# Kernel optimization log

Measured on AMD Instinct MI355X. Metric: run time of the kernel, lower is better.

Reference implementation:

```python
import jax, jax.numpy as jnp
import numpy as np

N, E, IN, H, O, ED = 20000, 100000, 167, 4, 256, 10
HID = H * O  # 1024
BN_EPS = 1e-5


def _bn(x, g, b):
    # BatchNorm1d in training mode: batch statistics over nodes
    mu = x.mean(0)
    var = x.var(0)
    return (x - mu) * jax.lax.rsqrt(var + BN_EPS) * g + b


def _gat(x, src, dst, ef, Wg, We, attn, at, cb, heads, out):
    # modified_GAT: multi-head attention with edge features + time scalar
    n = x.shape[0]
    h = (x @ Wg).reshape(n, heads, out)                 # [N,H,O]
    e = (ef[:, 1:] @ We).reshape(-1, heads, out)        # [E,H,O] edge-feature proj
    t = ef[:, 0]                                        # [E] time feature
    # node-level attention scores (avoids materializing [E,H,O] twice)
    s_src = jnp.einsum('nhd,hd->nh', h, attn[0])
    s_dst = jnp.einsum('nhd,hd->nh', h, attn[1])
    s_e = jnp.einsum('ehd,hd->eh', e, attn[2])
    logits = jax.nn.leaky_relu(s_src[src] + s_dst[dst] + s_e + t[:, None] * at, 0.2)  # [E,H]
    # attention normalization: softmax over incoming edges of each dst node
    m = jax.ops.segment_max(logits, dst, num_segments=n)
    m = jnp.where(jnp.isfinite(m), m, 0.0)
    p = jnp.exp(logits - m[dst])
    denom = jax.ops.segment_sum(p, dst, num_segments=n)
    w = p / (denom[dst] + 1e-16)                        # [E,H]
    msg = w[:, :, None] * (h[src] + e)                  # [E,H,O]
    agg = jax.ops.segment_sum(msg, dst, num_segments=n) # [N,H,O]
    return agg.reshape(n, heads * out) + cb


def setup_inputs() -> dict:
    key = jax.random.key(0)
    ks = iter(jax.random.split(key, 64))

    def nrm(shape, s):
        return jax.random.normal(next(ks), shape, dtype=jnp.float32) * np.float32(s)

    d = {}
    d['x'] = jax.random.normal(next(ks), (N, IN), dtype=jnp.float32)
    d['edge_index'] = jax.random.randint(next(ks), (2, E), 0, N)
    d['edge_attr'] = jax.random.uniform(next(ks), (E, ED + 2), dtype=jnp.float32)
    conv_dims = [(IN, H, O), (HID, H, O), (HID, 1, 2)]
    for i, (fin, hh, oo) in enumerate(conv_dims, 1):
        d[f'Wg{i}'] = nrm((fin, hh * oo), 1.0 / np.sqrt(fin))
        d[f'We{i}'] = nrm((ED, hh * oo), 1.0 / np.sqrt(ED))
        d[f'attn{i}'] = nrm((3, hh, oo), 0.1)
        d[f'at{i}'] = nrm((hh,), 0.1)
        d[f'cb{i}'] = jnp.zeros((hh * oo,), jnp.float32)
    lin_dims = [(IN, HID), (HID, HID), (HID, 2)]
    bn_dims = [IN, HID, HID]
    for i, (fin, fo) in enumerate(lin_dims, 1):
        d[f'lw{i}'] = nrm((fin, fo), 1.0 / np.sqrt(fin))
        d[f'lb{i}'] = jnp.zeros((fo,), jnp.float32)
        d[f'g{i}'] = jnp.ones((bn_dims[i - 1],), jnp.float32)
        d[f'b{i}'] = jnp.zeros((bn_dims[i - 1],), jnp.float32)
    return d


def reference(x, edge_index, edge_attr,
              Wg1, We1, attn1, at1, cb1, lw1, lb1, g1, b1,
              Wg2, We2, attn2, at2, cb2, lw2, lb2, g2, b2,
              Wg3, We3, attn3, at3, cb3, lw3, lb3, g3, b3):
    src, dst = edge_index[0], edge_index[1]
    ef = edge_attr[:, :-1]  # drop edge class column
    h = _bn(x, g1, b1)
    h = jax.nn.relu(h @ lw1 + lb1 + _gat(h, src, dst, ef, Wg1, We1, attn1, at1, cb1, H, O))
    h = _bn(h, g2, b2)
    h = jax.nn.relu(h @ lw2 + lb2 + _gat(h, src, dst, ef, Wg2, We2, attn2, at2, cb2, H, O))
    h = _bn(h, g3, b3)
    h = jax.nn.relu(h @ lw3 + lb3 + _gat(h, src, dst, ef, Wg3, We3, attn3, at3, cb3, 1, 2))
    return h
```

## Files before the change

kernel.cpp:

```cpp
#include <hip/hip_runtime.h>
#include <math.h>

#define NN 20000
#define EE 100000
#define FIN 167
#define KP1 256
#define HID 1024
#define OO 256
#define NB 16

typedef unsigned short u16;
typedef short bf16x8 __attribute__((ext_vector_type(8)));
typedef short s16x4  __attribute__((ext_vector_type(4)));
typedef float f32x4  __attribute__((ext_vector_type(4)));

__device__ __forceinline__ float bf(u16 u){ return __uint_as_float(((unsigned)u)<<16); }
__device__ __forceinline__ u16 fb(float v){
  unsigned u = __float_as_uint(v);
  return (u16)((u + 0x7FFFu + ((u>>16)&1u)) >> 16);
}
__device__ __forceinline__ float ldv(const float* p, long i){ return p[i]; }
__device__ __forceinline__ float ldv(const u16*   p, long i){ return bf(p[i]); }

__global__ void k_count(const int* __restrict__ ei, int* __restrict__ counts){
  int e = blockIdx.x*256 + threadIdx.x;
  if (e < EE) atomicAdd(&counts[ei[EE+e]], 1);
}

__global__ __launch_bounds__(256) void k_scan(const int* __restrict__ counts, int* __restrict__ iptr){
  __shared__ int sd[256];
  int tid = threadIdx.x;
  int carry = 0;
  for (int base=0; base<NN; base+=256){
    int i = base+tid;
    int v = (i<NN)? counts[i] : 0;
    sd[tid]=v;
    __syncthreads();
    for (int off=1; off<256; off<<=1){
      int t = (tid>=off)? sd[tid-off] : 0;
      __syncthreads();
      sd[tid] += t;
      __syncthreads();
    }
    if (i<NN) iptr[i] = carry + sd[tid] - v;
    carry += sd[255];
    __syncthreads();
  }
  if (tid==0) iptr[NN]=carry;
}

__global__ void k_fill(const int* __restrict__ ei, const int* __restrict__ iptr,
                       int* __restrict__ cursor, int* __restrict__ eid){
  int e = blockIdx.x*256 + threadIdx.x;
  if (e < EE){
    int d = ei[EE+e];
    int pos = atomicAdd(&cursor[d],1);
    eid[iptr[d]+pos] = e;
  }
}

template<typename T>
__global__ void k_bnstats(const T* __restrict__ X, float* __restrict__ sums, int F){
  int f = blockIdx.y*256 + threadIdx.x;
  if (f >= F) return;
  int r0 = blockIdx.x*100, r1 = r0+100;
  float s=0.f, s2=0.f;
  for (int r=r0;r<r1;r++){ float v = ldv(X,(long)r*F+f); s += v; s2 += v*v; }
  atomicAdd(&sums[f], s);
  atomicAdd(&sums[F+f], s2);
}

__global__ __launch_bounds__(256) void k_bnstats8(const u16* __restrict__ X, float* __restrict__ part){
  int tid = threadIdx.x;
  int f8 = (tid & 127)*8;
  int r0 = blockIdx.x*79, r1 = min(NN, r0+79);
  float s[8]={0,0,0,0,0,0,0,0}, s2[8]={0,0,0,0,0,0,0,0};
  for (int r=r0 + (tid>>7); r<r1; r+=2){
    bf16x8 v = *(const bf16x8*)(X + (long)r*HID + f8);
    #pragma unroll
    for (int j=0;j<8;j++){ float x=bf((u16)v[j]); s[j]+=x; s2[j]+=x*x; }
  }
  __shared__ float red[256][8];
  float* pb = part + (long)blockIdx.x*2048;
  #pragma unroll
  for (int j=0;j<8;j++) red[tid][j]=s[j];
  __syncthreads();
  if (tid<128){
    #pragma unroll
    for (int j=0;j<8;j++) pb[f8+j] = red[tid][j]+red[tid+128][j];
  }
  __syncthreads();
  #pragma unroll
  for (int j=0;j<8;j++) red[tid][j]=s2[j];
  __syncthreads();
  if (tid<128){
    #pragma unroll
    for (int j=0;j<8;j++) pb[1024+f8+j] = red[tid][j]+red[tid+128][j];
  }
}

__global__ __launch_bounds__(256) void k_pred(const float* __restrict__ part, float* __restrict__ sums){
  int idx = blockIdx.x*256 + threadIdx.x;
  float s = 0.f;
  #pragma unroll 8
  for (int b=0;b<256;b++) s += part[(long)b*2048 + idx];
  sums[idx] = s;
}

__global__ void k_bnfin(const float* __restrict__ sums, const float* __restrict__ g,
                        const float* __restrict__ b, float* __restrict__ scale,
                        float* __restrict__ shift, int F){
  int f = blockIdx.x*256 + threadIdx.x;
  if (f >= F) return;
  float mu  = sums[f]   * (1.f/NN);
  float var = sums[F+f] * (1.f/NN) - mu*mu;
  float sc  = rsqrtf(var + 1e-5f) * g[f];
  scale[f] = sc;
  shift[f] = b[f] - mu*sc;
}

__global__ __launch_bounds__(256) void k_foldT(const float* __restrict__ Wg, const float* __restrict__ Wl,
                        const float* __restrict__ scale,
                        u16* __restrict__ Wt, int K, int Kp){
  __shared__ float t[32][33];
  int k0 = blockIdx.x*32, c0 = blockIdx.y*32;
  int tx = threadIdx.x & 31, ty = threadIdx.x >> 5;
  bool second = (c0 >= HID);
  const float* W = second ? Wl : Wg;
  int cc0 = second ? c0 - HID : c0;
  #pragma unroll
  for (int i=0;i<4;i++){
    int k = k0 + ty + i*8;
    t[ty+i*8][tx] = (k < K) ? W[(long)k*HID + cc0 + tx] * scale[k] : 0.f;
  }
  __syncthreads();
  #pragma unroll
  for (int i=0;i<4;i++){
    int c = c0 + ty + i*8;
    Wt[(long)c*Kp + k0 + tx] = fb(t[tx][ty+i*8]);
  }
}

__global__ void k_cinit(const float* __restrict__ lb, float* __restrict__ cst){
  int c = blockIdx.x*256 + threadIdx.x;
  if (c < 2*HID) cst[c] = (c >= HID) ? lb[c-HID] : 0.f;
}

__global__ __launch_bounds__(256) void k_const(const float* __restrict__ Wg, const float* __restrict__ Wl,
                        const float* __restrict__ shift, float* __restrict__ cst, int K){
  int tx = threadIdx.x & 63, ty = threadIdx.x >> 6;
  int c = blockIdx.x*64 + tx;
  bool second = c >= HID;
  const float* W = second ? Wl : Wg;
  int cc = second ? c-HID : c;
  int k0 = blockIdx.y*128;
  int k1 = min(K, k0+128);
  float s = 0.f;
  for (int k=k0+ty; k<k1; k+=4) s += shift[k]*W[(long)k*HID+cc];
  __shared__ float red[256];
  red[threadIdx.x] = s;
  __syncthreads();
  if (ty == 0){
    float tot = red[tx] + red[tx+64] + red[tx+128] + red[tx+192];
    atomicAdd(&cst[c], tot);
  }
}

__global__ void k_cast(const float* __restrict__ x, u16* __restrict__ xb){
  long idx = (long)blockIdx.x*256 + threadIdx.x;
  if (idx >= (long)NN*KP1) return;
  int n = (int)(idx / KP1), k = (int)(idx % KP1);
  xb[idx] = (k<FIN)? fb(x[(long)n*FIN+k]) : (u16)0;
}

__global__ void k_we16(const float* __restrict__ We, u16* __restrict__ We16){
  int i = blockIdx.x*256 + threadIdx.x;
  if (i < 10*HID) We16[i] = fb(We[i]);
}

#define MF(a_,b_,c_) __builtin_amdgcn_mfma_f32_16x16x32_bf16(a_,b_,c_,0,0,0)
#define FENCE asm volatile("" ::: "memory")
#define BAR do { FENCE; __builtin_amdgcn_s_barrier(); FENCE; } while(0)

__global__ __launch_bounds__(512,2) void k_gemm(const u16* __restrict__ A, int K,
                     const u16* __restrict__ Wt, const float* __restrict__ cst,
                     u16* __restrict__ Chg, u16* __restrict__ Clin){
  __shared__ u16 lds[2][24576];
  int b = blockIdx.x;
  int wg = (b & 7)*158 + (b >> 3);
  int row0 = (wg >> 4)*256, col0 = (wg & 15)*128;
  int tid = threadIdx.x;
  int wave = tid >> 6, lane = tid & 63, quad = lane >> 4, lo = lane & 15;
  int wm = wave >> 1, wn = wave & 1;
  const u16* Apt[2];
  #pragma unroll
  for (int i=0;i<2;i++){
    int s = i*512 + tid, srow = s>>2;
    int gr = row0 + srow; if (gr >= NN) gr = NN-1;
    Apt[i] = A + (long)gr*K + (((s&3)^(srow&3))*8);
  }
  int brow = tid>>2;
  const u16* Bpt = Wt + (long)(col0 + brow)*K + ((((tid&3)^(brow&3)))*8);
  const char* ldsc = (const char*)&lds[0][0];
  int axor = lo & 3;
  int aoff = (wm*64 + lo)*64 + ((quad^axor)*16);
  int boff = 32768 + (wn*64 + lo)*64 + ((quad^axor)*16);
  int NT = K >> 6;
  f32x4 acc[4][4] = {};
  {
    u16* d = (u16*)&lds[0][0];
    __builtin_amdgcn_global_load_lds(Apt[0],      d +          tid*8, 16, 0, 0);
    __builtin_amdgcn_global_load_lds(Apt[1],      d +  4096 +  tid*8, 16, 0, 0);
    __builtin_amdgcn_global_load_lds(Bpt,         d + 16384 +  tid*8, 16, 0, 0);
    __builtin_amdgcn_global_load_lds(Apt[0] + 32, d +  8192 +  tid*8, 16, 0, 0);
    __builtin_amdgcn_global_load_lds(Apt[1] + 32, d + 12288 +  tid*8, 16, 0, 0);
    __builtin_amdgcn_global_load_lds(Bpt    + 32, d + 20480 +  tid*8, 16, 0, 0);
    asm volatile("s_waitcnt vmcnt(3)" ::: "memory");
    BAR;
  }
  for (int t=0; t<NT; t++){
    const char* Lb = ldsc + (t&1)*49152;
    u16* Sb = (u16*)&lds[0][0] + ((t&1)^1)*24576;
    int k0n = (t+1) << 6;
    int nx = (t+1 < NT);
    bf16x8 af[4], bfr[4];
    #pragma unroll
    for (int i=0;i<4;i++) af[i]  = *(const bf16x8*)(Lb + aoff + i*1024);
    #pragma unroll
    for (int n=0;n<4;n++) bfr[n] = *(const bf16x8*)(Lb + boff + n*1024);
    if (nx){
      __builtin_amdgcn_global_load_lds(Apt[0] + k0n, Sb +          tid*8, 16, 0, 0);
      __builtin_amdgcn_global_load_lds(Apt[1] + k0n, Sb +  4096 +  tid*8, 16, 0, 0);
      __builtin_amdgcn_global_load_lds(Bpt    + k0n, Sb + 16384 +  tid*8, 16, 0, 0);
    }
    #pragma unroll
    for (int i=0;i<4;i++)
      #pragma unroll
      for (int n=0;n<4;n++)
        acc[i][n] = MF(af[i], bfr[n], acc[i][n]);
    if (nx) asm volatile("s_waitcnt vmcnt(3)" ::: "memory");
    else    asm volatile("s_waitcnt vmcnt(0)" ::: "memory");
    BAR;
    #pragma unroll
    for (int i=0;i<4;i++) af[i]  = *(const bf16x8*)(Lb + 16384 + aoff + i*1024);
    #pragma unroll
    for (int n=0;n<4;n++) bfr[n] = *(const bf16x8*)(Lb +  8192 + boff + n*1024);
    if (nx){
      __builtin_amdgcn_global_load_lds(Apt[0] + k0n + 32, Sb +  8192 +  tid*8, 16, 0, 0);
      __builtin_amdgcn_global_load_lds(Apt[1] + k0n + 32, Sb + 12288 +  tid*8, 16, 0, 0);
      __builtin_amdgcn_global_load_lds(Bpt    + k0n + 32, Sb + 20480 +  tid*8, 16, 0, 0);
    }
    #pragma unroll
    for (int i=0;i<4;i++)
      #pragma unroll
      for (int n=0;n<4;n++)
        acc[i][n] = MF(af[i], bfr[n], acc[i][n]);
    if (nx) asm volatile("s_waitcnt vmcnt(3)" ::: "memory");
    BAR;
  }
  #pragma unroll
  for (int i=0;i<4;i++){
    #pragma unroll
    for (int n=0;n<4;n++){
      int col = col0 + wn*64 + n*16 + lo;
      float cs = cst[col];
      #pragma unroll
      for (int r=0;r<4;r++){
        int row = row0 + wm*64 + i*16 + quad*4 + r;
        if (row < NN){
          u16 o = fb(acc[i][n][r] + cs);
          if (col < HID) Chg[(long)row*HID + col] = o;
          else           Clin[(long)row*HID + col - HID] = o;
        }
      }
    }
  }
}
#undef MF
#undef BAR
#undef FENCE

__global__ __launch_bounds__(256) void k_sdot(const u16* __restrict__ hg, const float* __restrict__ attn,
                       float* __restrict__ ssrc, float* __restrict__ sdst){
  int unit = blockIdx.x*4 + (threadIdx.x >> 6);
  if (unit >= NN*4) return;
  int lane = threadIdx.x & 63;
  int n = unit >> 2, h = unit & 3;
  const u16* hp = hg + (long)n*HID + h*OO + lane*4;
  s16x4 v = *(const s16x4*)hp;
  float4 x0 = *(const float4*)(attn + h*OO + lane*4);
  float4 x1 = *(const float4*)(attn + HID + h*OO + lane*4);
  float f0 = bf((u16)v.x), f1 = bf((u16)v.y), f2 = bf((u16)v.z), f3 = bf((u16)v.w);
  float ss = f0*x0.x + f1*x0.y + f2*x0.z + f3*x0.w;
  float sd = f0*x1.x + f1*x1.y + f2*x1.z + f3*x1.w;
  #pragma unroll
  for (int off=32; off>0; off>>=1){
    ss += __shfl_down(ss, off);
    sd += __shfl_down(sd, off);
  }
  if (lane==0){ ssrc[unit]=ss; sdst[unit]=sd; }
}

__global__ void k_q(const float* __restrict__ We, const float* __restrict__ attn,
                    float* __restrict__ q){
  int t = threadIdx.x;
  if (t >= 40) return;
  int k = t >> 2, h = t & 3;
  float s = 0.f;
  for (int d=0; d<OO; d++) s += We[(long)k*HID + h*OO + d] * attn[2*HID + h*OO + d];
  q[k*4+h] = s;
}

__global__ void k_logits(const int* __restrict__ ei, const float* __restrict__ ea,
                         const float* __restrict__ q, const float* __restrict__ at,
                         const float* __restrict__ ssrc, const float* __restrict__ sdst,
                         float* __restrict__ L){
  int e = blockIdx.x*256 + threadIdx.x;
  if (e >= EE) return;
  int s = ei[e], dd = ei[EE+e];
  float4 a0 = *(const float4*)(ea + (long)e*12);
  float4 a1 = *(const float4*)(ea + (long)e*12 + 4);
  float4 a2 = *(const float4*)(ea + (long)e*12 + 8);
  float t = a0.x;
  float cc[10] = {a0.y,a0.z,a0.w, a1.x,a1.y,a1.z,a1.w, a2.x,a2.y,a2.z};
  float4 ss = *(const float4*)(ssrc + (long)s*4);
  float4 sd = *(const float4*)(sdst + (long)dd*4);
  float sv[4] = {ss.x+sd.x, ss.y+sd.y, ss.z+sd.z, ss.w+sd.w};
  float4 out;
  #pragma unroll
  for (int h=0;h<4;h++){
    float se = 0.f;
    #pragma unroll
    for (int k=0;k<10;k++) se += cc[k]*q[k*4+h];
    float v = sv[h] + se + t*at[h];
    ((float*)&out)[h] = (v>0.f)? v : 0.2f*v;
  }
  *(float4*)(L + (long)e*4) = out;
}

__global__ void k_mden(const int* __restrict__ iptr, const int* __restrict__ eid,
                       const float* __restrict__ ea, float* __restrict__ L,
                       float* __restrict__ cw){
  int n = blockIdx.x*256 + threadIdx.x;
  if (n >= NN) return;
  int b = iptr[n], e1 = iptr[n+1];
  float m0=-INFINITY, m1=-INFINITY, m2=-INFINITY, m3=-INFINITY;
  for (int i=b;i<e1;i++){
    float4 l = *(const float4*)(L + (long)eid[i]*4);
    m0=fmaxf(m0,l.x); m1=fmaxf(m1,l.y); m2=fmaxf(m2,l.z); m3=fmaxf(m3,l.w);
  }
  if (b==e1){ m0=m1=m2=m3=0.f; }
  float s0=0.f,s1=0.f,s2=0.f,s3=0.f;
  for (int i=b;i<e1;i++){
    float4 l = *(const float4*)(L + (long)eid[i]*4);
    s0+=expf(l.x-m0); s1+=expf(l.y-m1); s2+=expf(l.z-m2); s3+=expf(l.w-m3);
  }
  float d0=1.f/(s0+1e-16f), d1=1.f/(s1+1e-16f), d2=1.f/(s2+1e-16f), d3=1.f/(s3+1e-16f);
  float c[4][10] = {};
  for (int i=b;i<e1;i++){
    int e = eid[i];
    float4 l = *(const float4*)(L + (long)e*4);
    float4 w = { expf(l.x-m0)*d0, expf(l.y-m1)*d1, expf(l.z-m2)*d2, expf(l.w-m3)*d3 };
    *(float4*)(L + (long)e*4) = w;
    float4 a0 = *(const float4*)(ea + (long)e*12);
    float4 a1 = *(const float4*)(ea + (long)e*12 + 4);
    float4 a2 = *(const float4*)(ea + (long)e*12 + 8);
    float cc[10] = {a0.y,a0.z,a0.w, a1.x,a1.y,a1.z,a1.w, a2.x,a2.y,a2.z};
    #pragma unroll
    for (int k=0;k<10;k++){
      c[0][k] += w.x*cc[k]; c[1][k] += w.y*cc[k];
      c[2][k] += w.z*cc[k]; c[3][k] += w.w*cc[k];
    }
  }
  float* cp = cw + (long)n*40;
  #pragma unroll
  for (int h=0;h<4;h++)
    #pragma unroll
    for (int k=0;k<10;k++) cp[h*10+k] = c[h][k];
}

__global__ __launch_bounds__(256) void k_gath(
    const u16* __restrict__ hg, const int* __restrict__ ei,
    const int* __restrict__ iptr, const int* __restrict__ eid,
    const float* __restrict__ L,
    const float* __restrict__ cw,
    const u16* __restrict__ We16, const float* __restrict__ cb,
    u16* __restrict__ lio)
{
  __shared__ u16  sWe[10*HID];
  __shared__ float scb[HID];
  int tid = threadIdx.x;
  for (int i=tid;i<10*HID;i+=256) sWe[i] = We16[i];
  for (int i=tid;i<HID;i+=256) scb[i] = cb[i];
  __syncthreads();
  int h = tid >> 6;
  int f0 = tid*4;
  int d0 = blockIdx.x*NB, dend = min(NN, d0+NB);
  for (int d=d0; d<dend; d++){
    s16x4 a0 = *(const s16x4*)(lio + (long)d*HID + f0);
    float acc0=bf((u16)a0.x), acc1=bf((u16)a0.y), acc2=bf((u16)a0.z), acc3=bf((u16)a0.w);
    int b0 = iptr[d], en = iptr[d+1];
    for (int i=b0;i<en;i++){
      int e = eid[i], s_ = ei[e];
      float w = L[(long)e*4 + h];
      s16x4 v = *(const s16x4*)(hg + (long)s_*HID + f0);
      acc0 += w*bf((u16)v.x); acc1 += w*bf((u16)v.y);
      acc2 += w*bf((u16)v.z); acc3 += w*bf((u16)v.w);
    }
    const float* cp = cw + (long)d*40 + h*10;
    float ew0=0.f, ew1=0.f, ew2=0.f, ew3=0.f;
    #pragma unroll
    for (int k=0;k<10;k++){
      float c = cp[k];
      s16x4 wv = *(const s16x4*)(sWe + k*HID + f0);
      ew0 += c*bf((u16)wv.x); ew1 += c*bf((u16)wv.y);
      ew2 += c*bf((u16)wv.z); ew3 += c*bf((u16)wv.w);
    }
    acc0 += ew0; acc1 += ew1; acc2 += ew2; acc3 += ew3;
    u16 o[4];
    o[0] = fb(fmaxf(acc0 + scb[f0  ], 0.f));
    o[1] = fb(fmaxf(acc1 + scb[f0+1], 0.f));
    o[2] = fb(fmaxf(acc2 + scb[f0+2], 0.f));
    o[3] = fb(fmaxf(acc3 + scb[f0+3], 0.f));
    *(s16x4*)(lio + (long)d*HID + f0) = *(const s16x4*)o;
  }
}

__global__ void k_c4init(const float* __restrict__ lb, float* __restrict__ c4){
  if (threadIdx.x==0 && blockIdx.x==0){ c4[0]=0.f; c4[1]=0.f; c4[2]=lb[0]; c4[3]=lb[1]; }
}

__global__ __launch_bounds__(256) void k_fold3(const float* __restrict__ Wg, const float* __restrict__ lw,
                        const float* __restrict__ scale, const float* __restrict__ shift,
                        float* __restrict__ W4, float* __restrict__ c4){
  int k = blockIdx.x*256 + threadIdx.x;
  float sc = scale[k], sh = shift[k];
  float w0=Wg[k*2], w1=Wg[k*2+1], l0=lw[k*2], l1=lw[k*2+1];
  float4 o = {w0*sc, w1*sc, l0*sc, l1*sc};
  *(float4*)(W4 + (long)k*4) = o;
  __shared__ float red[256][4];
  int tid = threadIdx.x;
  red[tid][0]=sh*w0; red[tid][1]=sh*w1; red[tid][2]=sh*l0; red[tid][3]=sh*l1;
  __syncthreads();
  for (int o2=128;o2>0;o2>>=1){
    if (tid<o2){
      #pragma unroll
      for (int j=0;j<4;j++) red[tid][j]+=red[tid+o2][j];
    }
    __syncthreads();
  }
  if (tid==0){
    #pragma unroll
    for (int j=0;j<4;j++) atomicAdd(&c4[j], red[0][j]);
  }
}

__global__ __launch_bounds__(256) void k_n3(const u16* __restrict__ in,
    const float* __restrict__ W4, const float* __restrict__ c4,
    const float* __restrict__ attn,
    float* __restrict__ hg3, float* __restrict__ lin3,
    float* __restrict__ ssrc, float* __restrict__ sdst)
{
  __shared__ float sW[HID*4];
  __shared__ float sx[4][HID];
  int tid = threadIdx.x;
  int n0 = blockIdx.x*4;
  for (int i=tid; i<HID; i+=256) *(float4*)&sW[i*4] = *(const float4*)(W4 + (long)i*4);
  for (int idx=tid; idx<512; idx+=256){
    int rr = idx>>7, ch = idx&127;
    bf16x8 v = *(const bf16x8*)(in + (long)(n0+rr)*HID + ch*8);
    #pragma unroll
    for (int j=0;j<8;j++) sx[rr][ch*8+j] = bf((u16)v[j]);
  }
  __syncthreads();
  int w = tid>>6, lane = tid&63;
  float p0=0.f,p1=0.f,p2=0.f,p3=0.f;
  #pragma unroll
  for (int g=0; g<16; g++){
    int k = g*64 + lane;
    float x = sx[w][k];
    float4 wv = *(const float4*)&sW[k*4];
    p0 += x*wv.x; p1 += x*wv.y; p2 += x*wv.z; p3 += x*wv.w;
  }
  #pragma unroll
  for (int off=32; off>0; off>>=1){
    p0 += __shfl_down(p0, off);
    p1 += __shfl_down(p1, off);
    p2 += __shfl_down(p2, off);
    p3 += __shfl_down(p3, off);
  }
  if (lane==0){
    int n = n0 + w;
    float r0=p0+c4[0], r1=p1+c4[1], r2=p2+c4[2], r3=p3+c4[3];
    hg3[n*2]=r0; hg3[n*2+1]=r1;
    lin3[n*2]=r2; lin3[n*2+1]=r3;
    ssrc[n]=r0*attn[0]+r1*attn[1];
    sdst[n]=r0*attn[2]+r1*attn[3];
  }
}

__global__ void k_logits3(const int* __restrict__ ei, const float* __restrict__ ea,
                          const float* __restrict__ We, const float* __restrict__ attn,
                          const float* __restrict__ at, const float* __restrict__ ssrc,
                          const float* __restrict__ sdst, float* __restrict__ L){
  int e = blockIdx.x*256 + threadIdx.x;
  if (e >= EE) return;
  int s = ei[e], d = ei[EE+e];
  float e0=0.f, e1=0.f;
  #pragma unroll
  for (int k=0;k<10;k++){
    float c = ea[e*12+1+k];
    e0 += c*We[k*2]; e1 += c*We[k*2+1];
  }
  float se = e0*attn[4] + e1*attn[5];
  float v = ssrc[s] + sdst[d] + se + ea[e*12]*at[0];
  L[e] = (v>0.f)? v : 0.2f*v;
}

__global__ void k_mden3(const int* __restrict__ iptr, const int* __restrict__ eid,
                        const float* __restrict__ ea, float* __restrict__ L,
                        float* __restrict__ cw){
  int n = blockIdx.x*256 + threadIdx.x;
  if (n >= NN) return;
  int b = iptr[n], e1 = iptr[n+1];
  float mx = -INFINITY;
  for (int i=b;i<e1;i++) mx = fmaxf(mx, L[eid[i]]);
  if (b == e1) mx = 0.f;
  float s = 0.f;
  for (int i=b;i<e1;i++) s += expf(L[eid[i]] - mx);
  float dv = 1.f/(s+1e-16f);
  float c[10] = {0.f,0.f,0.f,0.f,0.f,0.f,0.f,0.f,0.f,0.f};
  for (int i=b;i<e1;i++){
    int e = eid[i];
    float w = expf(L[e]-mx)*dv;
    L[e] = w;
    #pragma unroll
    for (int k=0;k<10;k++) c[k] += w*ea[e*12+1+k];
  }
  float* cp = cw + (long)n*10;
  #pragma unroll
  for (int k=0;k<10;k++) cp[k] = c[k];
}

__global__ void k_gather3(const int* __restrict__ ei,
                          const int* __restrict__ iptr, const int* __restrict__ eid,
                          const float* __restrict__ L,
                          const float* __restrict__ cw,
                          const float* __restrict__ hg3,
                          const float* __restrict__ We, const float* __restrict__ lin3,
                          const float* __restrict__ cb, float* __restrict__ out){
  int n = blockIdx.x*256 + threadIdx.x;
  if (n >= NN) return;
  int b = iptr[n], en = iptr[n+1];
  const float* cp = cw + (long)n*10;
  float e0f=0.f, e1f=0.f;
  #pragma unroll
  for (int k=0;k<10;k++){ e0f += cp[k]*We[k*2]; e1f += cp[k]*We[k*2+1]; }
  float a0=0.f, a1=0.f;
  for (int i=b;i<en;i++){
    int e = eid[i], s_ = ei[e];
    float w = L[e];
    a0 += w*hg3[s_*2];
    a1 += w*hg3[s_*2+1];
  }
  out[n*2]   = fmaxf(lin3[n*2]  +a0+e0f+cb[0], 0.f);
  out[n*2+1] = fmaxf(lin3[n*2+1]+a1+e1f+cb[1], 0.f);
}

extern "C" void kernel_launch(void* const* d_in, const int* in_sizes, int n_in,
                              void* d_out, int out_size, void* d_ws, size_t ws_size,
                              hipStream_t stream){
  const int* ei = (const int*)d_in[1];

  long long sz[64];
  {
    const long long* s64 = (const long long*)(const void*)in_sizes;
    bool is64 = (n_in >= 2) && (in_sizes[0] == 3340000) && (in_sizes[1] == 0)
                && (s64[1] == 200000);
    for (int i=0;i<n_in && i<64;i++) sz[i] = is64 ? s64[i] : (long long)in_sizes[i];
  }

  int IWg[3], IWe[3], IAttn[3], IAt[3], ICb[3], ILw[3], ILb[3], IG[3], IB[3];
  if (n_in > 8 && sz[8] == (long long)HID*HID){
    for (int l=0;l<3;l++){
      IWg[l]=3+l*5; IWe[l]=4+l*5; IAttn[l]=5+l*5; IAt[l]=6+l*5; ICb[l]=7+l*5;
      ILw[l]=18+l*4; ILb[l]=19+l*4; IG[l]=20+l*4; IB[l]=21+l*4;
    }
  } else {
    int idx=3;
    for (int l=0;l<3;l++){
      IWg[l]=idx++; IWe[l]=idx++; IAttn[l]=idx++; IAt[l]=idx++; ICb[l]=idx++;
      ILw[l]=idx++; ILb[l]=idx++; IG[l]=idx++; IB[l]=idx++;
    }
  }
  #define FP(i) ((const float*)d_in[(i)])

  char* ws = (char*)d_ws;
  size_t off = 0;
  auto alloc = [&](size_t bytes)->void*{ void* p = ws + off; off += (bytes + 255) & ~(size_t)255; return p; };
  auto G = [](long n){ return (int)((n+255)/256); };

  u16*   buf0 = (u16*)  alloc((size_t)NN*HID*2);
  u16*   bufA = (u16*)  alloc((size_t)NN*HID*2);
  u16*   bufB = (u16*)  alloc((size_t)NN*HID*2);
  u16*   xbf  = (u16*)  alloc((size_t)NN*KP1*2);
  u16*   Wt   = (u16*)  alloc((size_t)2*HID*HID*2);
  u16*   We16 = (u16*)  alloc((size_t)10*HID*2);
  float* cst  = (float*)alloc(2*HID*4);
  float* L    = (float*)alloc((size_t)EE*4*4);
  float* ssrc = (float*)alloc((size_t)NN*4*4);
  float* sdst = (float*)alloc((size_t)NN*4*4);
  int*   iptr = (int*)  alloc((size_t)(NN+4)*4);
  int*   cnts = (int*)  alloc((size_t)NN*4);
  int*   eid  = (int*)  alloc((size_t)EE*4);
  float* stats= (float*)alloc(2*HID*4);
  float* scale= (float*)alloc(HID*4);
  float* shift= (float*)alloc(HID*4);
  float* qbuf = (float*)alloc(64*4);
  float* hg3  = (float*)alloc((size_t)NN*2*4);
  float* lin3 = (float*)alloc((size_t)NN*2*4);
  float* cw   = (float*)alloc((size_t)NN*40*4);
  float* W4   = (float*)alloc((size_t)HID*4*4);
  float* c4   = (float*)alloc(4*4);
  float* part = (float*)alloc((size_t)256*2048*4);

  hipMemsetAsync(cnts, 0, NN*sizeof(int), stream);
  k_count<<<G(EE),256,0,stream>>>(ei, cnts);
  k_scan<<<1,256,0,stream>>>(cnts, iptr);
  hipMemsetAsync(cnts, 0, NN*sizeof(int), stream);
  k_fill<<<G(EE),256,0,stream>>>(ei, iptr, cnts, eid);

  int gg = 1264;
  int gsd = (NN*4+3)/4;

  {
    hipMemsetAsync(stats, 0, 2*FIN*sizeof(float), stream);
    dim3 bg(200, 1);
    k_bnstats<float><<<bg,256,0,stream>>>(FP(0), stats, FIN);
    k_bnfin<<<1,256,0,stream>>>(stats, FP(IG[0]), FP(IB[0]), scale, shift, FIN);
    k_cast<<<G((long)NN*KP1),256,0,stream>>>(FP(0), xbf);
    dim3 ft(KP1/32, 64);
    k_foldT<<<ft,256,0,stream>>>(FP(IWg[0]), FP(ILw[0]), scale, Wt, FIN, KP1);
    k_cinit<<<8,256,0,stream>>>(FP(ILb[0]), cst);
    dim3 cg(32, (FIN+127)/128);
    k_const<<<cg,256,0,stream>>>(FP(IWg[0]), FP(ILw[0]), shift, cst, FIN);
    k_we16<<<40,256,0,stream>>>(FP(IWe[0]), We16);
    k_gemm<<<gg,512,0,stream>>>(xbf, KP1, Wt, cst, buf0, bufA);
    k_sdot<<<gsd,256,0,stream>>>(buf0, FP(IAttn[0]), ssrc, sdst);
    k_q<<<1,64,0,stream>>>(FP(IWe[0]), FP(IAttn[0]), qbuf);
    k_logits<<<G(EE),256,0,stream>>>(ei, FP(2), qbuf, FP(IAt[0]), ssrc, sdst, L);
    k_mden<<<G(NN),256,0,stream>>>(iptr, eid, FP(2), L, cw);
    k_gath<<<(NN+NB-1)/NB,256,0,stream>>>(buf0, ei, iptr, eid, L, cw,
                                          We16, FP(ICb[0]), bufA);
  }
  {
    k_bnstats8<<<256,256,0,stream>>>(bufA, part);
    k_pred<<<8,256,0,stream>>>(part, stats);
    k_bnfin<<<4,256,0,stream>>>(stats, FP(IG[1]), FP(IB[1]), scale, shift, HID);
    dim3 ft(HID/32, 64);
    k_foldT<<<ft,256,0,stream>>>(FP(IWg[1]), FP(ILw[1]), scale, Wt, HID, HID);
    k_cinit<<<8,256,0,stream>>>(FP(ILb[1]), cst);
    dim3 cg(32, HID/128);
    k_const<<<cg,256,0,stream>>>(FP(IWg[1]), FP(ILw[1]), shift, cst, HID);
    k_we16<<<40,256,0,stream>>>(FP(IWe[1]), We16);
    k_gemm<<<gg,512,0,stream>>>(bufA, HID, Wt, cst, buf0, bufB);
    k_sdot<<<gsd,256,0,stream>>>(buf0, FP(IAttn[1]), ssrc, sdst);
    k_q<<<1,64,0,stream>>>(FP(IWe[1]), FP(IAttn[1]), qbuf);
    k_logits<<<G(EE),256,0,stream>>>(ei, FP(2), qbuf, FP(IAt[1]), ssrc, sdst, L);
    k_mden<<<G(NN),256,0,stream>>>(iptr, eid, FP(2), L, cw);
    k_gath<<<(NN+NB-1)/NB,256,0,stream>>>(buf0, ei, iptr, eid, L, cw,
                                          We16, FP(ICb[1]), bufB);
  }

  k_bnstats8<<<256,256,0,stream>>>(bufB, part);
  k_pred<<<8,256,0,stream>>>(part, stats);
  k_bnfin<<<4,256,0,stream>>>(stats, FP(IG[2]), FP(IB[2]), scale, shift, HID);
  k_c4init<<<1,64,0,stream>>>(FP(ILb[2]), c4);
  k_fold3<<<HID/256,256,0,stream>>>(FP(IWg[2]), FP(ILw[2]), scale, shift, W4, c4);
  k_n3<<<NN/4,256,0,stream>>>(bufB, W4, c4, FP(IAttn[2]), hg3, lin3, ssrc, sdst);
  k_logits3<<<G(EE),256,0,stream>>>(ei, FP(2), FP(IWe[2]), FP(IAttn[2]), FP(IAt[2]), ssrc, sdst, L);
  k_mden3<<<G(NN),256,0,stream>>>(iptr, eid, FP(2), L, cw);
  k_gather3<<<G(NN),256,0,stream>>>(ei, iptr, eid, L, cw, hg3,
                                    FP(IWe[2]), lin3, FP(ICb[2]), (float*)d_out);
}
```

Measured before the change: 891.0 us.

## Parallelize CSR prefix scan, prefetch next edge in aggregation, halve nodes per block

Replaces the single-block serial prefix scan over node degrees with a three-kernel block-parallel scan (per-block scan, scan of block sums, offset add). In the GAT aggregation kernel, the next edge's weight and source feature row are software-prefetched while the current edge is accumulated, to hide gather latency. Nodes per block drops from 16 to 8 to create more blocks. The extra kernel launches and register use from prefetching trade against shorter serial chains.

```diff
diff --git a/kernel.cpp b/kernel.cpp
--- a/kernel.cpp
+++ b/kernel.cpp
@@ -7,7 +7,7 @@
 #define KP1 256
 #define HID 1024
 #define OO 256
-#define NB 16
+#define NB 8
 
 typedef unsigned short u16;
 typedef short bf16x8 __attribute__((ext_vector_type(8)));
@@ -27,26 +27,41 @@
   if (e < EE) atomicAdd(&counts[ei[EE+e]], 1);
 }
 
-__global__ __launch_bounds__(256) void k_scan(const int* __restrict__ counts, int* __restrict__ iptr){
+__global__ __launch_bounds__(256) void k_scanA(const int* __restrict__ counts,
+                                               int* __restrict__ iptr, int* __restrict__ bsum){
   __shared__ int sd[256];
-  int tid = threadIdx.x;
-  int carry = 0;
-  for (int base=0; base<NN; base+=256){
-    int i = base+tid;
-    int v = (i<NN)? counts[i] : 0;
-    sd[tid]=v;
+  int b = blockIdx.x, tid = threadIdx.x;
+  int i = b*256 + tid;
+  int v = (i<NN)? counts[i] : 0;
+  sd[tid]=v; __syncthreads();
+  for (int off=1; off<256; off<<=1){
+    int t = (tid>=off)? sd[tid-off] : 0;
     __syncthreads();
-    for (int off=1; off<256; off<<=1){
-      int t = (tid>=off)? sd[tid-off] : 0;
-      __syncthreads();
-      sd[tid] += t;
-      __syncthreads();
-    }
-    if (i<NN) iptr[i] = carry + sd[tid] - v;
-    carry += sd[255];
+    sd[tid] += t;
     __syncthreads();
   }
-  if (tid==0) iptr[NN]=carry;
+  if (i<NN) iptr[i] = sd[tid]-v;
+  if (tid==255) bsum[b]=sd[255];
+}
+__global__ __launch_bounds__(128) void k_scanB(const int* __restrict__ bsum,
+                                               int* __restrict__ boff, int* __restrict__ iptrN,
+                                               int nb){
+  __shared__ int sd[128];
+  int tid=threadIdx.x;
+  int v=(tid<nb)? bsum[tid]:0;
+  sd[tid]=v; __syncthreads();
+  for (int off=1; off<128; off<<=1){
+    int t=(tid>=off)?sd[tid-off]:0;
+    __syncthreads();
+    sd[tid]+=t;
+    __syncthreads();
+  }
+  if (tid<nb) boff[tid]=sd[tid]-v;
+  if (tid==127) *iptrN = sd[127];
+}
+__global__ void k_scanC(const int* __restrict__ boff, int* __restrict__ iptr){
+  int i = blockIdx.x*256+threadIdx.x;
+  if (i<NN) iptr[i] += boff[blockIdx.x];
 }
 
 __global__ void k_fill(const int* __restrict__ ei, const int* __restrict__ iptr,
@@ -400,10 +415,19 @@
     s16x4 a0 = *(const s16x4*)(lio + (long)d*HID + f0);
     float acc0=bf((u16)a0.x), acc1=bf((u16)a0.y), acc2=bf((u16)a0.z), acc3=bf((u16)a0.w);
     int b0 = iptr[d], en = iptr[d+1];
+    float wN = 0.f; s16x4 vN = {};
+    if (b0 < en){
+      int e = eid[b0], s_ = ei[e];
+      wN = L[(long)e*4 + h];
+      vN = *(const s16x4*)(hg + (long)s_*HID + f0);
+    }
     for (int i=b0;i<en;i++){
-      int e = eid[i], s_ = ei[e];
-      float w = L[(long)e*4 + h];
-      s16x4 v = *(const s16x4*)(hg + (long)s_*HID + f0);
+      float w = wN; s16x4 v = vN;
+      if (i+1 < en){
+        int e2 = eid[i+1], s2 = ei[e2];
+        wN = L[(long)e2*4 + h];
+        vN = *(const s16x4*)(hg + (long)s2*HID + f0);
+      }
       acc0 += w*bf((u16)v.x); acc1 += w*bf((u16)v.y);
       acc2 += w*bf((u16)v.z); acc3 += w*bf((u16)v.w);
     }
@@ -613,6 +637,8 @@
   int*   iptr = (int*)  alloc((size_t)(NN+4)*4);
   int*   cnts = (int*)  alloc((size_t)NN*4);
   int*   eid  = (int*)  alloc((size_t)EE*4);
+  int*   bsum = (int*)  alloc(256*4);
+  int*   boff = (int*)  alloc(256*4);
   float* stats= (float*)alloc(2*HID*4);
   float* scale= (float*)alloc(HID*4);
   float* shift= (float*)alloc(HID*4);
@@ -624,9 +650,12 @@
   float* c4   = (float*)alloc(4*4);
   float* part = (float*)alloc((size_t)256*2048*4);
 
+  int nsb = G(NN);
   hipMemsetAsync(cnts, 0, NN*sizeof(int), stream);
   k_count<<<G(EE),256,0,stream>>>(ei, cnts);
-  k_scan<<<1,256,0,stream>>>(cnts, iptr);
+  k_scanA<<<nsb,256,0,stream>>>(cnts, iptr, bsum);
+  k_scanB<<<1,128,0,stream>>>(bsum, boff, iptr+NN, nsb);
+  k_scanC<<<nsb,256,0,stream>>>(boff, iptr);
   hipMemsetAsync(cnts, 0, NN*sizeof(int), stream);
   k_fill<<<G(EE),256,0,stream>>>(ei, iptr, cnts, eid);
 
```

Result: faster. 815.3 us (-8.5%).
